# Performance work log

Measured on AMD Instinct MI355X. Metric: run time of the kernel, lower is better.

The kernel has to match this reference:

```python
import jax, jax.numpy as jnp
import numpy as np

B, SL, RATIO = 2, 2048, 16
SG = SL // RATIO          # 128 global tokens
S = SL + SG               # 2176 total sequence
D, H, NC, V = 512, 8, 2, 32000
HD, FF = D // H, 2 * D    # head_dim=64, dim_feedforward=2*d_model
K, R = 4, 4               # rel_pos_max_distance, local_attention_radius
NEG = -1e9


def _ln(x, g, b):
    m = x.mean(-1, keepdims=True)
    v = ((x - m) ** 2).mean(-1, keepdims=True)
    return (x - m) * jax.lax.rsqrt(v + 1e-5) * g + b


def _forward(token_ids, embed, global_token, rel_bias, q_w, q_b, k_w, k_b,
             v_w, v_b, o_w, o_b, ln1_g, ln1_b, ln2_g, ln2_b,
             ff1_w, ff1_b, ff2_w, ff2_b, cls_w1, cls_w2):
    pad = token_ids == 0                                   # B x Sl (padding_idx=0)
    x_long = embed[token_ids]                              # B x Sl x D
    seg_pad = pad.reshape(B, SG, RATIO).all(-1)            # B x Sg: segment fully padded
    x_global = jnp.broadcast_to(global_token, (B, SG, D))  # learned auxiliary global token
    x = jnp.concatenate([x_long, x_global], axis=1)        # B x S x D
    pad_all = jnp.concatenate([pad, seg_pad], axis=1)      # B x S

    # --- global-local attention structure (static masks) ---
    pos = jnp.arange(S)
    is_long = pos < SL
    both_long = is_long[:, None] & is_long[None, :]
    dist = pos[None, :] - pos[:, None]
    # long<->long restricted to local window; any pair involving a global token is allowed
    allowed = jnp.where(both_long, jnp.abs(dist) <= R, True)          # S x S
    rel = jnp.clip(dist, -K, K) + K                                   # S x S in [0, 2K]
    bias = jnp.where(both_long[None], rel_bias[:, rel], 0.0)          # H x S x S

    def heads(t):
        return t.reshape(B, S, H, HD).transpose(0, 2, 1, 3)           # B x H x S x hd
    q = heads(x @ q_w + q_b)
    k = heads(x @ k_w + k_b)
    v = heads(x @ v_w + v_b)
    logits = jnp.einsum('bhid,bhjd->bhij', q, k) / np.float32(np.sqrt(HD)) + bias[None]
    logits = jnp.where(allowed[None, None], logits, NEG)
    logits = jnp.where(pad_all[:, None, None, :], NEG, logits)        # key padding mask
    attn = jax.nn.softmax(logits, axis=-1)
    o = jnp.einsum('bhij,bhjd->bhid', attn, v).transpose(0, 2, 1, 3).reshape(B, S, D)

    # post-norm TransformerEncoderLayer (dropout=0, activation=relu)
    x = _ln(x + (o @ o_w + o_b), ln1_g, ln1_b)
    ff = jax.nn.relu(x @ ff1_w + ff1_b) @ ff2_w + ff2_b
    x = _ln(x + ff, ln2_g, ln2_b)

    # masked mean over global tokens, then MLP head
    zg = x[:, SL:, :]                                                 # B x Sg x D
    zg = jnp.where(seg_pad[..., None], 0.0, zg).sum(1) / (~seg_pad).sum(1, keepdims=True)
    return jax.nn.relu(zg @ cls_w1) @ cls_w2                          # B x Nc


def setup_inputs() -> dict:
    key = jax.random.key(0)
    ks = jax.random.split(key, 16)
    s = 0.02
    embed = jax.random.normal(ks[0], (V, D)) * s
    embed = embed.at[0].set(0.0)  # padding_idx row
    return {
        'x_long_token_ids': jax.random.randint(ks[1], (B, SL), 0, V),
        'embed': embed,
        'global_token': jax.random.normal(ks[2], (D,)) * s,
        'rel_bias': jax.random.normal(ks[3], (H, 2 * K + 1)) * s,
        'q_w': jax.random.normal(ks[4], (D, D)) * s, 'q_b': jnp.zeros((D,)),
        'k_w': jax.random.normal(ks[5], (D, D)) * s, 'k_b': jnp.zeros((D,)),
        'v_w': jax.random.normal(ks[6], (D, D)) * s, 'v_b': jnp.zeros((D,)),
        'o_w': jax.random.normal(ks[7], (D, D)) * s, 'o_b': jnp.zeros((D,)),
        'ln1_g': jnp.ones((D,)), 'ln1_b': jnp.zeros((D,)),
        'ln2_g': jnp.ones((D,)), 'ln2_b': jnp.zeros((D,)),
        'ff1_w': jax.random.normal(ks[8], (D, FF)) * s, 'ff1_b': jnp.zeros((FF,)),
        'ff2_w': jax.random.normal(ks[9], (FF, D)) * s, 'ff2_b': jnp.zeros((D,)),
        'cls_w1': jax.random.normal(ks[10], (D, D // 2)) * s,
        'cls_w2': jax.random.normal(ks[11], (D // 2, NC)) * s,
    }


def reference(x_long_token_ids, embed, global_token, rel_bias, q_w, q_b, k_w, k_b,
              v_w, v_b, o_w, o_b, ln1_g, ln1_b, ln2_g, ln2_b,
              ff1_w, ff1_b, ff2_w, ff2_b, cls_w1, cls_w2):
    return _forward(x_long_token_ids, embed, global_token, rel_bias, q_w, q_b,
                    k_w, k_b, v_w, v_b, o_w, o_b, ln1_g, ln1_b, ln2_g, ln2_b,
                    ff1_w, ff1_b, ff2_w, ff2_b, cls_w1, cls_w2)
```

## Files before the change

kernel.cpp:

```cpp
#include <hip/hip_runtime.h>
#include <hip/hip_bf16.h>
#include <cstddef>

#define B_ 2
#define SL_ 2048
#define RATIO_ 16
#define SG_ 128
#define S_ 2176
#define D_ 512
#define H_ 8
#define HD_ 64
#define FF_ 1024
#define NC_ 2
#define NEG_ (-1.0e9f)
#define MINF_ (-1.0e30f)
#define MROWS_ (B_ * S_)
#define GR_ (B_ * SG_)
#define KC_ 8

typedef __attribute__((ext_vector_type(8))) short short8;
typedef __attribute__((ext_vector_type(4))) float f32x4;

__device__ __forceinline__ void gll16(const void* g, void* l) {
    __builtin_amdgcn_global_load_lds((const __attribute__((address_space(1))) void*)g,
                                     (__attribute__((address_space(3))) void*)l, 16, 0, 0);
}
__device__ __forceinline__ unsigned short f2bf(float x) {
    __hip_bfloat16 h = __float2bfloat16(x);
    return *reinterpret_cast<unsigned short*>(&h);
}
__device__ __forceinline__ float wave_sum(float v) {
#pragma unroll
    for (int off = 1; off < 64; off <<= 1) v += __shfl_xor(v, off);
    return v;
}
#define BARRIER() do { asm volatile("" ::: "memory"); __builtin_amdgcn_s_barrier(); asm volatile("" ::: "memory"); } while (0)

__global__ void build_x_kernel(const int* __restrict__ ids,
                               const float* __restrict__ embed,
                               const float* __restrict__ gtok,
                               __hip_bfloat16* __restrict__ xb,
                               float* __restrict__ xg,
                               int* __restrict__ pad_all) {
    int row = blockIdx.x;
    int b = row / S_, s = row % S_;
    const float* src;
    if (s < SL_) {
        int tok = ids[b * SL_ + s];
        src = embed + (size_t)tok * D_;
        if (threadIdx.x == 0) pad_all[row] = (tok == 0) ? 1 : 0;
    } else {
        src = gtok;
        if (threadIdx.x == 0) {
            int g = s - SL_;
            int allz = 1;
            for (int r = 0; r < RATIO_; ++r)
                allz &= (ids[b * SL_ + g * RATIO_ + r] == 0) ? 1 : 0;
            pad_all[row] = allz;
        }
    }
    float4 v = ((const float4*)src)[threadIdx.x];
    __hip_bfloat16 hb[4] = {__float2bfloat16(v.x), __float2bfloat16(v.y),
                            __float2bfloat16(v.z), __float2bfloat16(v.w)};
    *(uint2*)(xb + (size_t)row * D_ + threadIdx.x * 4) = *(const uint2*)hb;
    if (s >= SL_)
        ((float4*)(xg + (size_t)(b * SG_ + s - SL_) * D_))[threadIdx.x] = v;
}

__global__ __launch_bounds__(256) void wt_all_kernel(const float* __restrict__ qw,
                                                     const float* __restrict__ kw,
                                                     const float* __restrict__ vw,
                                                     const float* __restrict__ ow,
                                                     const float* __restrict__ f1w,
                                                     const float* __restrict__ f2w,
                                                     __hip_bfloat16* __restrict__ WqT,
                                                     __hip_bfloat16* __restrict__ WkvT,
                                                     __hip_bfloat16* __restrict__ WoT,
                                                     __hip_bfloat16* __restrict__ W1T,
                                                     __hip_bfloat16* __restrict__ W2T,
                                                     const float* __restrict__ k_b,
                                                     const float* __restrict__ v_b,
                                                     float* __restrict__ kvb) {
    __shared__ float tile[64][65];
    int bid = blockIdx.x;
    int tid = threadIdx.x;
    if (bid == 0) {
#pragma unroll
        for (int i = tid; i < 1024; i += 256)
            kvb[i] = (i < 512) ? k_b[i] : v_b[i - 512];
    }
    const float* W; __hip_bfloat16* Wt; int K, N, tx, ty;
    if (bid < 192) {
        int which = bid >> 6, id = bid & 63;
        W = (which == 0) ? qw : (which == 1) ? kw : vw;
        Wt = (which == 0) ? WqT : (which == 1) ? WkvT : (WkvT + (size_t)512 * 512);
        K = 512; N = 512; tx = id & 7; ty = id >> 3;
    } else if (bid < 256) {
        int id = bid - 192; W = ow; Wt = WoT; K = 512; N = 512; tx = id & 7; ty = id >> 3;
    } else if (bid < 384) {
        int id = bid - 256; W = f1w; Wt = W1T; K = 512; N = 1024; tx = id & 15; ty = id >> 4;
    } else {
        int id = bid - 384; W = f2w; Wt = W2T; K = 1024; N = 512; tx = id & 7; ty = id >> 3;
    }
    int n0 = tx * 64, k0 = ty * 64;
    int c = tid & 63, r4 = tid >> 6;
#pragma unroll
    for (int i = 0; i < 16; ++i) {
        int r = i * 4 + r4;
        tile[r][c] = W[(size_t)(k0 + r) * N + n0 + c];
    }
    __syncthreads();
#pragma unroll
    for (int i = 0; i < 16; ++i) {
        int n = i * 4 + r4;
        Wt[(size_t)(n0 + n) * K + k0 + c] = __float2bfloat16(tile[c][n]);
    }
}

__global__ __launch_bounds__(256) void gemm_bt_kernel(const __hip_bfloat16* __restrict__ A,
                                                      const __hip_bfloat16* __restrict__ Bt,
                                                      const float* __restrict__ bias,
                                                      void* __restrict__ Cout,
                                                      int N, int K, int flags) {
    __shared__ short As[2][128 * 32];
    __shared__ short Bs[2][128 * 32];
    int tid = threadIdx.x;
    int m0 = blockIdx.y * 128, n0 = blockIdx.x * 128;
    int w = tid >> 6, lane = tid & 63;
    int wr = w >> 1, wc = w & 1;

    f32x4 acc[4][4];
#pragma unroll
    for (int m = 0; m < 4; ++m)
#pragma unroll
        for (int n = 0; n < 4; ++n)
            acc[m][n] = (f32x4){0.f, 0.f, 0.f, 0.f};

    int p0 = tid * 16, rs = p0 >> 6, cs = p0 & 63;
    const char* Ab = (const char*)A;
    const char* Bb = (const char*)Bt;

    auto STAGE = [&](int buf, int k0) {
        gll16(Ab + ((size_t)(m0 + rs) * K + k0) * 2 + cs, (char*)As[buf] + p0);
        gll16(Ab + ((size_t)(m0 + rs + 64) * K + k0) * 2 + cs, (char*)As[buf] + p0 + 4096);
        gll16(Bb + ((size_t)(n0 + rs) * K + k0) * 2 + cs, (char*)Bs[buf] + p0);
        gll16(Bb + ((size_t)(n0 + rs + 64) * K + k0) * 2 + cs, (char*)Bs[buf] + p0 + 4096);
    };
    STAGE(0, 0);
    int nk = K >> 5;
    for (int t = 0; t < nk; ++t) {
        int cur = t & 1;
        if (t + 1 < nk) {
            STAGE(cur ^ 1, (t + 1) << 5);
            asm volatile("s_waitcnt vmcnt(4)" ::: "memory");
        } else {
            asm volatile("s_waitcnt vmcnt(0)" ::: "memory");
        }
        BARRIER();
        short8 af[4], bfr[4];
#pragma unroll
        for (int m = 0; m < 4; ++m)
            af[m] = *(const short8*)&As[cur][(wr * 64 + m * 16 + (lane & 15)) * 32 + (lane >> 4) * 8];
#pragma unroll
        for (int n = 0; n < 4; ++n)
            bfr[n] = *(const short8*)&Bs[cur][(wc * 64 + n * 16 + (lane & 15)) * 32 + (lane >> 4) * 8];
#pragma unroll
        for (int m = 0; m < 4; ++m)
#pragma unroll
            for (int n = 0; n < 4; ++n)
                acc[m][n] = __builtin_amdgcn_mfma_f32_16x16x32_bf16(af[m], bfr[n], acc[m][n], 0, 0, 0);
        BARRIER();
    }

    int rbase = m0 + wr * 64 + (lane >> 4) * 4;
    int cbase = n0 + wc * 64 + (lane & 15);
#pragma unroll
    for (int m = 0; m < 4; ++m)
#pragma unroll
        for (int n = 0; n < 4; ++n) {
            int col = cbase + n * 16;
            float bv = bias[col];
#pragma unroll
            for (int j = 0; j < 4; ++j) {
                int row = rbase + m * 16 + j;
                float v = acc[m][n][j] + bv;
                if (flags & 1) v = fmaxf(v, 0.0f);
                if (flags & 2)
                    ((__hip_bfloat16*)Cout)[(size_t)row * N + col] = __float2bfloat16(v);
                else
                    ((float*)Cout)[(size_t)row * N + col] = v;
            }
        }
}

__global__ __launch_bounds__(256) void gemm64_kernel(const __hip_bfloat16* __restrict__ A,
                                                     const __hip_bfloat16* __restrict__ Bt,
                                                     const float* __restrict__ bias,
                                                     const float* __restrict__ Res,
                                                     void* __restrict__ Cout,
                                                     int N, int K, int flags) {
    __shared__ short As[2][64 * 32];
    __shared__ short Bs[2][64 * 32];
    int tid = threadIdx.x;
    int m0 = blockIdx.y * 64, n0 = blockIdx.x * 64;
    int w = tid >> 6, lane = tid & 63;
    int wr = w >> 1, wc = w & 1;

    f32x4 acc[2][2];
#pragma unroll
    for (int m = 0; m < 2; ++m)
#pragma unroll
        for (int n = 0; n < 2; ++n)
            acc[m][n] = (f32x4){0.f, 0.f, 0.f, 0.f};

    int p0 = tid * 16, rs = p0 >> 6, cs = p0 & 63;
    int rl = m0 + rs;
    size_t arow = (flags & 8) ? (size_t)((rl >> 7) * S_ + SL_ + (rl & 127)) : (size_t)rl;
    const char* Ab = (const char*)A;
    const char* Bb = (const char*)Bt;

    auto STAGE = [&](int buf, int k0) {
        gll16(Ab + (arow * K + k0) * 2 + cs, (char*)As[buf] + p0);
        gll16(Bb + ((size_t)(n0 + rs) * K + k0) * 2 + cs, (char*)Bs[buf] + p0);
    };
    STAGE(0, 0);
    int nk = K >> 5;
    for (int t = 0; t < nk; ++t) {
        int cur = t & 1;
        if (t + 1 < nk) {
            STAGE(cur ^ 1, (t + 1) << 5);
            asm volatile("s_waitcnt vmcnt(2)" ::: "memory");
        } else {
            asm volatile("s_waitcnt vmcnt(0)" ::: "memory");
        }
        BARRIER();
        short8 af[2], bfr[2];
#pragma unroll
        for (int m = 0; m < 2; ++m)
            af[m] = *(const short8*)&As[cur][(wr * 32 + m * 16 + (lane & 15)) * 32 + (lane >> 4) * 8];
#pragma unroll
        for (int n = 0; n < 2; ++n)
            bfr[n] = *(const short8*)&Bs[cur][(wc * 32 + n * 16 + (lane & 15)) * 32 + (lane >> 4) * 8];
#pragma unroll
        for (int m = 0; m < 2; ++m)
#pragma unroll
            for (int n = 0; n < 2; ++n)
                acc[m][n] = __builtin_amdgcn_mfma_f32_16x16x32_bf16(af[m], bfr[n], acc[m][n], 0, 0, 0);
        BARRIER();
    }

    int rbase = m0 + wr * 32 + (lane >> 4) * 4;
    int cbase = n0 + wc * 32 + (lane & 15);
#pragma unroll
    for (int m = 0; m < 2; ++m)
#pragma unroll
        for (int n = 0; n < 2; ++n) {
            int col = cbase + n * 16;
            float bv = bias[col];
#pragma unroll
            for (int j = 0; j < 4; ++j) {
                int row = rbase + m * 16 + j;
                float v = acc[m][n][j] + bv;
                if (flags & 4) v += Res[(size_t)row * N + col];
                if (flags & 1) v = fmaxf(v, 0.0f);
                if (flags & 2)
                    ((__hip_bfloat16*)Cout)[(size_t)row * N + col] = __float2bfloat16(v);
                else
                    ((float*)Cout)[(size_t)row * N + col] = v;
            }
        }
}

#define ATT_LDS_ 28480

__global__ __launch_bounds__(256, 4) void attn_global_kernel(const __hip_bfloat16* __restrict__ Qg,
                                                             const __hip_bfloat16* __restrict__ KV,
                                                             const int* __restrict__ pad_all,
                                                             float* __restrict__ pacc,
                                                             float* __restrict__ pm,
                                                             float* __restrict__ pl) {
    __shared__ __align__(16) char smem[ATT_LDS_];
    short* Qs = (short*)(smem + 0);
    short* Ks = (short*)(smem + 4608);
    short* Vt = (short*)(smem + 13824);
    short* Pl = (short*)(smem + 23040);
    float* padv = (float*)(smem + 27648);
    float* msh  = (float*)(smem + 27968);
    float* lsh  = (float*)(smem + 28224);
    float* Osh  = (float*)smem;

    const int TS[KC_ + 1] = {0, 4, 8, 12, 17, 21, 25, 29, 34};
    int bid = blockIdx.x;
    int c  = bid & 7;
    int qt = (bid >> 3) & 3;
    int h  = (bid >> 5) & 7;
    int b  = bid >> 8;
    int i0c = qt * 32;
    int tid = threadIdx.x;
    int w = tid >> 6, lane = tid & 63;
    int qg = w >> 1, kh = w & 1;
    int cq = lane & 15, g4 = lane >> 4;
    const int* pad = pad_all + b * S_;
    const short* qgp = (const short*)Qg;
    const short* kv  = (const short*)KV;

    {
        int q = tid >> 3, g = tid & 7;
        short8 v = *(const short8*)(qgp + (size_t)(b * SG_ + i0c + q) * D_ + h * HD_ + g * 8);
        *(short8*)(Qs + q * 72 + g * 8) = v;
    }

    float mreg = MINF_, lreg = 0.0f;
    f32x4 ot0 = {0,0,0,0}, ot1 = {0,0,0,0}, ot2 = {0,0,0,0}, ot3 = {0,0,0,0};

    for (int t = TS[c]; t < TS[c + 1]; ++t) {
        int j0 = t * 64;
        __syncthreads();
        {
            int key = tid >> 2, g2 = tid & 3;
            size_t base = (size_t)(b * S_ + j0 + key) * 1024 + h * HD_;
#pragma unroll
            for (int gg = 0; gg < 2; ++gg) {
                int g = g2 + gg * 4;
                short8 kvv = *(const short8*)(kv + base + g * 8);
                *(short8*)(Ks + key * 72 + g * 8) = kvv;
                short8 vv = *(const short8*)(kv + base + 512 + g * 8);
#pragma unroll
                for (int i = 0; i < 8; ++i)
                    Vt[(g * 8 + i) * 72 + key] = vv[i];
            }
            if (tid < 64) padv[tid] = pad[j0 + tid] ? NEG_ : 0.0f;
        }
        __syncthreads();

        short8 qf0 = *(const short8*)(Qs + (qg * 16 + cq) * 72 + 0 + g4 * 8);
        short8 qf1 = *(const short8*)(Qs + (qg * 16 + cq) * 72 + 32 + g4 * 8);
        f32x4 st0 = {0,0,0,0}, st1 = {0,0,0,0};
        {
            short8 kf;
            kf = *(const short8*)(Ks + (kh * 32 + cq) * 72 + 0 + g4 * 8);
            st0 = __builtin_amdgcn_mfma_f32_16x16x32_bf16(kf, qf0, st0, 0, 0, 0);
            kf = *(const short8*)(Ks + (kh * 32 + cq) * 72 + 32 + g4 * 8);
            st0 = __builtin_amdgcn_mfma_f32_16x16x32_bf16(kf, qf1, st0, 0, 0, 0);
            kf = *(const short8*)(Ks + (kh * 32 + 16 + cq) * 72 + 0 + g4 * 8);
            st1 = __builtin_amdgcn_mfma_f32_16x16x32_bf16(kf, qf0, st1, 0, 0, 0);
            kf = *(const short8*)(Ks + (kh * 32 + 16 + cq) * 72 + 32 + g4 * 8);
            st1 = __builtin_amdgcn_mfma_f32_16x16x32_bf16(kf, qf1, st1, 0, 0, 0);
        }
        float sarr[8];
#pragma unroll
        for (int mt = 0; mt < 2; ++mt)
#pragma unroll
            for (int j = 0; j < 4; ++j) {
                int k = kh * 32 + mt * 16 + g4 * 4 + j;
                sarr[mt * 4 + j] = (mt ? st1[j] : st0[j]) * 0.125f + padv[k];
            }
        float cmax = sarr[0];
#pragma unroll
        for (int i = 1; i < 8; ++i) cmax = fmaxf(cmax, sarr[i]);
        cmax = fmaxf(cmax, __shfl_xor(cmax, 16));
        cmax = fmaxf(cmax, __shfl_xor(cmax, 32));
        float mnew = fmaxf(mreg, cmax);
        float fac = __expf(mreg - mnew);
        float parr[8], psum = 0.0f;
#pragma unroll
        for (int i = 0; i < 8; ++i) { parr[i] = __expf(sarr[i] - mnew); psum += parr[i]; }
        psum += __shfl_xor(psum, 16);
        psum += __shfl_xor(psum, 32);
        lreg = lreg * fac + psum;
        mreg = mnew;
        ot0 *= fac; ot1 *= fac; ot2 *= fac; ot3 *= fac;
#pragma unroll
        for (int mt = 0; mt < 2; ++mt) {
            unsigned int lo = (unsigned int)f2bf(parr[mt * 4 + 0]) | ((unsigned int)f2bf(parr[mt * 4 + 1]) << 16);
            unsigned int hi = (unsigned int)f2bf(parr[mt * 4 + 2]) | ((unsigned int)f2bf(parr[mt * 4 + 3]) << 16);
            unsigned int* dst = (unsigned int*)(Pl + (qg * 16 + cq) * 72 + kh * 32 + mt * 16 + g4 * 4);
            dst[0] = lo; dst[1] = hi;
        }
        short8 pf = *(const short8*)(Pl + (qg * 16 + cq) * 72 + kh * 32 + g4 * 8);
        {
            short8 vf;
            vf = *(const short8*)(Vt + (0 * 16 + cq) * 72 + kh * 32 + g4 * 8);
            ot0 = __builtin_amdgcn_mfma_f32_16x16x32_bf16(vf, pf, ot0, 0, 0, 0);
            vf = *(const short8*)(Vt + (1 * 16 + cq) * 72 + kh * 32 + g4 * 8);
            ot1 = __builtin_amdgcn_mfma_f32_16x16x32_bf16(vf, pf, ot1, 0, 0, 0);
            vf = *(const short8*)(Vt + (2 * 16 + cq) * 72 + kh * 32 + g4 * 8);
            ot2 = __builtin_amdgcn_mfma_f32_16x16x32_bf16(vf, pf, ot2, 0, 0, 0);
            vf = *(const short8*)(Vt + (3 * 16 + cq) * 72 + kh * 32 + g4 * 8);
            ot3 = __builtin_amdgcn_mfma_f32_16x16x32_bf16(vf, pf, ot3, 0, 0, 0);
        }
    }

    __syncthreads();
    if (g4 == 0) {
        msh[(qg * 2 + kh) * 16 + cq] = mreg;
        lsh[(qg * 2 + kh) * 16 + cq] = lreg;
    }
    __syncthreads();
    {
        float m0 = msh[(qg * 2 + 0) * 16 + cq], m1 = msh[(qg * 2 + 1) * 16 + cq];
        float Mm = fmaxf(m0, m1);
        float e_self = __expf(mreg - Mm);
        f32x4 o;
        o = ot0 * e_self; *(f32x4*)(Osh + ((qg * 2 + kh) * 16 + cq) * 68 + 0  + g4 * 4) = o;
        o = ot1 * e_self; *(f32x4*)(Osh + ((qg * 2 + kh) * 16 + cq) * 68 + 16 + g4 * 4) = o;
        o = ot2 * e_self; *(f32x4*)(Osh + ((qg * 2 + kh) * 16 + cq) * 68 + 32 + g4 * 4) = o;
        o = ot3 * e_self; *(f32x4*)(Osh + ((qg * 2 + kh) * 16 + cq) * 68 + 48 + g4 * 4) = o;
    }
    __syncthreads();
    {
        int q_all = tid >> 3, d0 = (tid & 7) * 8;
        int qg2 = q_all >> 4, ql = q_all & 15;
        float mm0 = msh[(qg2 * 2 + 0) * 16 + ql], mm1 = msh[(qg2 * 2 + 1) * 16 + ql];
        float MM = fmaxf(mm0, mm1);
        float lt = lsh[(qg2 * 2 + 0) * 16 + ql] * __expf(mm0 - MM) +
                   lsh[(qg2 * 2 + 1) * 16 + ql] * __expf(mm1 - MM);
        int prow = ((c * B_ + b) * H_ + h) * SG_ + qt * 32 + q_all;
#pragma unroll
        for (int i = 0; i < 8; ++i) {
            float a = Osh[((qg2 * 2 + 0) * 16 + ql) * 68 + d0 + i] +
                      Osh[((qg2 * 2 + 1) * 16 + ql) * 68 + d0 + i];
            pacc[(size_t)prow * HD_ + d0 + i] = a;
        }
        if ((tid & 7) == 0) { pm[prow] = MM; pl[prow] = lt; }
    }
}

__global__ __launch_bounds__(256) void attn_combine_kernel(const float* __restrict__ pacc,
                                                           const float* __restrict__ pm,
                                                           const float* __restrict__ pl,
                                                           __hip_bfloat16* __restrict__ Og) {
    int wave = (int)((blockIdx.x * (size_t)blockDim.x + threadIdx.x) >> 6);
    int lane = threadIdx.x & 63;
    int gq = wave & (SG_ - 1);
    int h  = (wave >> 7) & 7;
    int b  = wave >> 10;

    float M = MINF_;
#pragma unroll
    for (int c = 0; c < KC_; ++c) {
        int pidx = ((c * B_ + b) * H_ + h) * SG_ + gq;
        M = fmaxf(M, pm[pidx]);
    }
    float L = 0.0f, Ov = 0.0f;
#pragma unroll
    for (int c = 0; c < KC_; ++c) {
        int pidx = ((c * B_ + b) * H_ + h) * SG_ + gq;
        float e = __expf(pm[pidx] - M);
        L += pl[pidx] * e;
        Ov += pacc[(size_t)pidx * HD_ + lane] * e;
    }
    Og[(size_t)(b * SG_ + gq) * D_ + h * HD_ + lane] = __float2bfloat16(Ov / L);
}

__global__ __launch_bounds__(256) void ln_kernel(const float* __restrict__ A,
                                                 const float* __restrict__ g,
                                                 const float* __restrict__ be,
                                                 float* __restrict__ out,
                                                 __hip_bfloat16* __restrict__ outb,
                                                 int wb) {
    int row = blockIdx.x;
    int tid = threadIdx.x;
    size_t base = (size_t)row * D_;
    float x0 = A[base + tid];
    float x1 = A[base + tid + 256];
    float s1 = x0 + x1;
    float s2 = x0 * x0 + x1 * x1;
    for (int off = 1; off < 64; off <<= 1) {
        s1 += __shfl_xor(s1, off);
        s2 += __shfl_xor(s2, off);
    }
    __shared__ float ws1[4], ws2[4];
    int wid = tid >> 6;
    if ((tid & 63) == 0) { ws1[wid] = s1; ws2[wid] = s2; }
    __syncthreads();
    s1 = ws1[0] + ws1[1] + ws1[2] + ws1[3];
    s2 = ws2[0] + ws2[1] + ws2[2] + ws2[3];
    float mean = s1 * (1.0f / D_);
    float var  = s2 * (1.0f / D_) - mean * mean;
    float rstd = rsqrtf(var + 1e-5f);
    float o0 = (x0 - mean) * rstd * g[tid]       + be[tid];
    float o1 = (x1 - mean) * rstd * g[tid + 256] + be[tid + 256];
    out[base + tid]       = o0;
    out[base + tid + 256] = o1;
    if (wb) {
        outb[base + tid]       = __float2bfloat16(o0);
        outb[base + tid + 256] = __float2bfloat16(o1);
    }
}

__global__ __launch_bounds__(256) void cls_part_kernel(const float* __restrict__ x2g,
                                                       const int* __restrict__ pad_all,
                                                       const float* __restrict__ w1,
                                                       float* __restrict__ part) {
    int kc = blockIdx.x, b = blockIdx.y, tid = threadIdx.x;
    __shared__ float wrow[SG_];
    __shared__ float zpart[4][64];
    __shared__ float zgs[64];
    if (tid < SG_) wrow[tid] = pad_all[b * S_ + SL_ + tid] ? 0.0f : 1.0f;
    __syncthreads();

    int j = tid & 63, grp = tid >> 6;
    float a = 0.0f;
#pragma unroll 8
    for (int g = grp; g < SG_; g += 4)
        a = fmaf(wrow[g], x2g[(size_t)(b * SG_ + g) * D_ + kc * 64 + j], a);
    zpart[grp][j] = a;
    __syncthreads();
    if (tid < 64) {
        float cnt = 0.0f;
#pragma unroll 16
        for (int g = 0; g < SG_; ++g) cnt += wrow[g];
        zgs[tid] = (zpart[0][tid] + zpart[1][tid] + zpart[2][tid] + zpart[3][tid]) / cnt;
    }
    __syncthreads();

    float s = 0.0f;
#pragma unroll 8
    for (int d = 0; d < 64; ++d)
        s = fmaf(zgs[d], w1[(size_t)(kc * 64 + d) * 256 + tid], s);
    part[(b * 8 + kc) * 256 + tid] = s;
}

__global__ __launch_bounds__(256) void cls_fin_kernel(const float* __restrict__ part,
                                                      const float* __restrict__ w2,
                                                      float* __restrict__ out) {
    int b = blockIdx.x, n = threadIdx.x;
    float hsum = 0.0f;
#pragma unroll
    for (int kc = 0; kc < 8; ++kc) hsum += part[(b * 8 + kc) * 256 + n];
    hsum = fmaxf(hsum, 0.0f);
    float o0 = hsum * w2[(size_t)n * NC_ + 0];
    float o1 = hsum * w2[(size_t)n * NC_ + 1];
    o0 = wave_sum(o0);
    o1 = wave_sum(o1);
    __shared__ float r0[4], r1[4];
    if ((n & 63) == 0) { r0[n >> 6] = o0; r1[n >> 6] = o1; }
    __syncthreads();
    if (n == 0) {
        out[b * NC_ + 0] = r0[0] + r0[1] + r0[2] + r0[3];
        out[b * NC_ + 1] = r1[0] + r1[1] + r1[2] + r1[3];
    }
}

extern "C" void kernel_launch(void* const* d_in, const int* in_sizes, int n_in,
                              void* d_out, int out_size, void* d_ws, size_t ws_size,
                              hipStream_t stream) {
    const int*   ids    = (const int*)d_in[0];
    const float* embed  = (const float*)d_in[1];
    const float* gtok   = (const float*)d_in[2];
    const float* q_w    = (const float*)d_in[4];
    const float* q_b    = (const float*)d_in[5];
    const float* k_w    = (const float*)d_in[6];
    const float* k_b    = (const float*)d_in[7];
    const float* v_w    = (const float*)d_in[8];
    const float* v_b    = (const float*)d_in[9];
    const float* o_w    = (const float*)d_in[10];
    const float* o_b    = (const float*)d_in[11];
    const float* ln1_g  = (const float*)d_in[12];
    const float* ln1_b  = (const float*)d_in[13];
    const float* ln2_g  = (const float*)d_in[14];
    const float* ln2_b  = (const float*)d_in[15];
    const float* ff1_w  = (const float*)d_in[16];
    const float* ff1_b  = (const float*)d_in[17];
    const float* ff2_w  = (const float*)d_in[18];
    const float* ff2_b  = (const float*)d_in[19];
    const float* cls_w1 = (const float*)d_in[20];
    const float* cls_w2 = (const float*)d_in[21];

    char* ws = (char*)d_ws;
    __hip_bfloat16* x_b     = (__hip_bfloat16*)(ws + 0);
    __hip_bfloat16* kv_bf   = (__hip_bfloat16*)(ws + 4456448);
    __hip_bfloat16* qg_bf   = (__hip_bfloat16*)(ws + 13369344);
    __hip_bfloat16* og_bf   = (__hip_bfloat16*)(ws + 13631488);
    float*          xg_f32  = (float*)(ws + 13893632);
    float*          tmpA    = (float*)(ws + 14417920);
    float*          x1g     = (float*)(ws + 14942208);
    __hip_bfloat16* x1g_b   = (__hip_bfloat16*)(ws + 15466496);
    __hip_bfloat16* ffh_b   = (__hip_bfloat16*)(ws + 15728640);
    float*          tmpB    = (float*)(ws + 16252928);
    float*          x2g     = (float*)(ws + 16777216);
    __hip_bfloat16* WqT     = (__hip_bfloat16*)(ws + 17301504);
    __hip_bfloat16* WkvT    = (__hip_bfloat16*)(ws + 17825792);
    __hip_bfloat16* WoT     = (__hip_bfloat16*)(ws + 18874368);
    __hip_bfloat16* W1T     = (__hip_bfloat16*)(ws + 19398656);
    __hip_bfloat16* W2T     = (__hip_bfloat16*)(ws + 20447232);
    float*          kvb     = (float*)(ws + 21495808);
    int*            pad_all = (int*)(ws + 21499904);
    float*          pacc    = (float*)(ws + 21520384);
    float*          pm      = (float*)(ws + 25714688);
    float*          pl      = (float*)(ws + 25780224);
    float*          clspart = (float*)(ws + 25845760);

    build_x_kernel<<<MROWS_, 128, 0, stream>>>(ids, embed, gtok, x_b, xg_f32, pad_all);
    wt_all_kernel<<<512, 256, 0, stream>>>(q_w, k_w, v_w, o_w, ff1_w, ff2_w,
                                           WqT, WkvT, WoT, W1T, W2T, k_b, v_b, kvb);

    gemm_bt_kernel<<<dim3(8, 34), 256, 0, stream>>>(x_b, WkvT, kvb, kv_bf, 1024, 512, 2);
    gemm64_kernel<<<dim3(8, 4), 256, 0, stream>>>(x_b, WqT, q_b, nullptr, qg_bf, 512, 512, 2 | 8);

    attn_global_kernel<<<512, 256, 0, stream>>>(qg_bf, kv_bf, pad_all, pacc, pm, pl);
    attn_combine_kernel<<<512, 256, 0, stream>>>(pacc, pm, pl, og_bf);

    gemm64_kernel<<<dim3(8, 4), 256, 0, stream>>>(og_bf, WoT, o_b, xg_f32, tmpA, 512, 512, 4);
    ln_kernel<<<GR_, 256, 0, stream>>>(tmpA, ln1_g, ln1_b, x1g, x1g_b, 1);
    gemm64_kernel<<<dim3(16, 4), 256, 0, stream>>>(x1g_b, W1T, ff1_b, nullptr, ffh_b, 1024, 512, 1 | 2);
    gemm64_kernel<<<dim3(8, 4), 256, 0, stream>>>(ffh_b, W2T, ff2_b, x1g, tmpB, 512, 1024, 4);
    ln_kernel<<<GR_, 256, 0, stream>>>(tmpB, ln2_g, ln2_b, x2g, nullptr, 0);

    cls_part_kernel<<<dim3(8, B_), 256, 0, stream>>>(x2g, pad_all, cls_w1, clspart);
    cls_fin_kernel<<<B_, 256, 0, stream>>>(clspart, cls_w2, (float*)d_out);
}
```

Before: 102.1 us.

## Merge prep and QKV launches, fuse tail stages into one cooperative kernel

Merges the embedding build and the weight transpose into one prep kernel, and merges the KV and global-Q GEMMs into one launch. Replaces the seven tail launches (attention combine, O-proj, LN1, FF1, FF2, LN2, classifier part and final) with a single 64-block cooperative kernel that separates stages with grid syncs. The aim is to cut launch overhead and inter-kernel gaps across many tiny kernels. In exchange, the tail now runs on only 64 blocks, and each grid sync adds its own latency.

```diff
diff --git a/kernel.cpp b/kernel.cpp
--- a/kernel.cpp
+++ b/kernel.cpp
@@ -1,6 +1,9 @@
 #include <hip/hip_runtime.h>
 #include <hip/hip_bf16.h>
+#include <hip/hip_cooperative_groups.h>
 #include <cstddef>
+
+namespace cg = cooperative_groups;
 
 #define B_ 2
 #define SL_ 2048
@@ -36,71 +39,72 @@
 }
 #define BARRIER() do { asm volatile("" ::: "memory"); __builtin_amdgcn_s_barrier(); asm volatile("" ::: "memory"); } while (0)
 
-__global__ void build_x_kernel(const int* __restrict__ ids,
-                               const float* __restrict__ embed,
-                               const float* __restrict__ gtok,
-                               __hip_bfloat16* __restrict__ xb,
-                               float* __restrict__ xg,
-                               int* __restrict__ pad_all) {
-    int row = blockIdx.x;
-    int b = row / S_, s = row % S_;
-    const float* src;
-    if (s < SL_) {
-        int tok = ids[b * SL_ + s];
-        src = embed + (size_t)tok * D_;
-        if (threadIdx.x == 0) pad_all[row] = (tok == 0) ? 1 : 0;
-    } else {
-        src = gtok;
-        if (threadIdx.x == 0) {
-            int g = s - SL_;
-            int allz = 1;
-            for (int r = 0; r < RATIO_; ++r)
-                allz &= (ids[b * SL_ + g * RATIO_ + r] == 0) ? 1 : 0;
-            pad_all[row] = allz;
-        }
-    }
-    float4 v = ((const float4*)src)[threadIdx.x];
-    __hip_bfloat16 hb[4] = {__float2bfloat16(v.x), __float2bfloat16(v.y),
-                            __float2bfloat16(v.z), __float2bfloat16(v.w)};
-    *(uint2*)(xb + (size_t)row * D_ + threadIdx.x * 4) = *(const uint2*)hb;
-    if (s >= SL_)
-        ((float4*)(xg + (size_t)(b * SG_ + s - SL_) * D_))[threadIdx.x] = v;
-}
-
-__global__ __launch_bounds__(256) void wt_all_kernel(const float* __restrict__ qw,
-                                                     const float* __restrict__ kw,
-                                                     const float* __restrict__ vw,
-                                                     const float* __restrict__ ow,
-                                                     const float* __restrict__ f1w,
-                                                     const float* __restrict__ f2w,
-                                                     __hip_bfloat16* __restrict__ WqT,
-                                                     __hip_bfloat16* __restrict__ WkvT,
-                                                     __hip_bfloat16* __restrict__ WoT,
-                                                     __hip_bfloat16* __restrict__ W1T,
-                                                     __hip_bfloat16* __restrict__ W2T,
-                                                     const float* __restrict__ k_b,
-                                                     const float* __restrict__ v_b,
-                                                     float* __restrict__ kvb) {
+__global__ __launch_bounds__(256) void prep_kernel(const int* __restrict__ ids,
+                                                   const float* __restrict__ embed,
+                                                   const float* __restrict__ gtok,
+                                                   __hip_bfloat16* __restrict__ xb,
+                                                   float* __restrict__ xg,
+                                                   int* __restrict__ pad_all,
+                                                   const float* __restrict__ qw,
+                                                   const float* __restrict__ kw,
+                                                   const float* __restrict__ vw,
+                                                   const float* __restrict__ ow,
+                                                   const float* __restrict__ f1w,
+                                                   const float* __restrict__ f2w,
+                                                   __hip_bfloat16* __restrict__ WqT,
+                                                   __hip_bfloat16* __restrict__ WkvT,
+                                                   __hip_bfloat16* __restrict__ WoT,
+                                                   __hip_bfloat16* __restrict__ W1T,
+                                                   __hip_bfloat16* __restrict__ W2T,
+                                                   const float* __restrict__ k_b,
+                                                   const float* __restrict__ v_b,
+                                                   float* __restrict__ kvb) {
     __shared__ float tile[64][65];
-    int bid = blockIdx.x;
-    int tid = threadIdx.x;
-    if (bid == 0) {
-#pragma unroll
+    int bid = blockIdx.x, tid = threadIdx.x;
+    if (bid < 2176) {
+        int half = tid >> 7, lt = tid & 127;
+        int row = bid * 2 + half;
+        int b = row / S_, s = row % S_;
+        const float* src;
+        if (s < SL_) {
+            int tok = ids[b * SL_ + s];
+            src = embed + (size_t)tok * D_;
+            if (lt == 0) pad_all[row] = (tok == 0) ? 1 : 0;
+        } else {
+            src = gtok;
+            if (lt == 0) {
+                int g = s - SL_;
+                int allz = 1;
+                for (int r = 0; r < RATIO_; ++r)
+                    allz &= (ids[b * SL_ + g * RATIO_ + r] == 0) ? 1 : 0;
+                pad_all[row] = allz;
+            }
+        }
+        float4 v = ((const float4*)src)[lt];
+        __hip_bfloat16 hb[4] = {__float2bfloat16(v.x), __float2bfloat16(v.y),
+                                __float2bfloat16(v.z), __float2bfloat16(v.w)};
+        *(uint2*)(xb + (size_t)row * D_ + lt * 4) = *(const uint2*)hb;
+        if (s >= SL_)
+            ((float4*)(xg + (size_t)(b * SG_ + s - SL_) * D_))[lt] = v;
+        return;
+    }
+    int wbid = bid - 2176;
+    if (wbid == 0) {
         for (int i = tid; i < 1024; i += 256)
             kvb[i] = (i < 512) ? k_b[i] : v_b[i - 512];
     }
     const float* W; __hip_bfloat16* Wt; int K, N, tx, ty;
-    if (bid < 192) {
-        int which = bid >> 6, id = bid & 63;
+    if (wbid < 192) {
+        int which = wbid >> 6, id = wbid & 63;
         W = (which == 0) ? qw : (which == 1) ? kw : vw;
         Wt = (which == 0) ? WqT : (which == 1) ? WkvT : (WkvT + (size_t)512 * 512);
         K = 512; N = 512; tx = id & 7; ty = id >> 3;
-    } else if (bid < 256) {
-        int id = bid - 192; W = ow; Wt = WoT; K = 512; N = 512; tx = id & 7; ty = id >> 3;
-    } else if (bid < 384) {
-        int id = bid - 256; W = f1w; Wt = W1T; K = 512; N = 1024; tx = id & 15; ty = id >> 4;
+    } else if (wbid < 256) {
+        int id = wbid - 192; W = ow; Wt = WoT; K = 512; N = 512; tx = id & 7; ty = id >> 3;
+    } else if (wbid < 384) {
+        int id = wbid - 256; W = f1w; Wt = W1T; K = 512; N = 1024; tx = id & 15; ty = id >> 4;
     } else {
-        int id = bid - 384; W = f2w; Wt = W2T; K = 1024; N = 512; tx = id & 7; ty = id >> 3;
+        int id = wbid - 384; W = f2w; Wt = W2T; K = 1024; N = 512; tx = id & 7; ty = id >> 3;
     }
     int n0 = tx * 64, k0 = ty * 64;
     int c = tid & 63, r4 = tid >> 6;
@@ -117,158 +121,132 @@
     }
 }
 
-__global__ __launch_bounds__(256) void gemm_bt_kernel(const __hip_bfloat16* __restrict__ A,
-                                                      const __hip_bfloat16* __restrict__ Bt,
-                                                      const float* __restrict__ bias,
-                                                      void* __restrict__ Cout,
-                                                      int N, int K, int flags) {
-    __shared__ short As[2][128 * 32];
-    __shared__ short Bs[2][128 * 32];
-    int tid = threadIdx.x;
-    int m0 = blockIdx.y * 128, n0 = blockIdx.x * 128;
+__global__ __launch_bounds__(256) void qkv_kernel(const __hip_bfloat16* __restrict__ x_b,
+                                                  const __hip_bfloat16* __restrict__ WkvT,
+                                                  const float* __restrict__ kvb,
+                                                  __hip_bfloat16* __restrict__ kv_bf,
+                                                  const __hip_bfloat16* __restrict__ WqT,
+                                                  const float* __restrict__ q_b,
+                                                  __hip_bfloat16* __restrict__ qg_bf) {
+    __shared__ short SA[2][4096];
+    __shared__ short SB[2][4096];
+    int bid = blockIdx.x, tid = threadIdx.x;
     int w = tid >> 6, lane = tid & 63;
     int wr = w >> 1, wc = w & 1;
-
-    f32x4 acc[4][4];
-#pragma unroll
-    for (int m = 0; m < 4; ++m)
-#pragma unroll
-        for (int n = 0; n < 4; ++n)
-            acc[m][n] = (f32x4){0.f, 0.f, 0.f, 0.f};
-
     int p0 = tid * 16, rs = p0 >> 6, cs = p0 & 63;
-    const char* Ab = (const char*)A;
-    const char* Bb = (const char*)Bt;
-
-    auto STAGE = [&](int buf, int k0) {
-        gll16(Ab + ((size_t)(m0 + rs) * K + k0) * 2 + cs, (char*)As[buf] + p0);
-        gll16(Ab + ((size_t)(m0 + rs + 64) * K + k0) * 2 + cs, (char*)As[buf] + p0 + 4096);
-        gll16(Bb + ((size_t)(n0 + rs) * K + k0) * 2 + cs, (char*)Bs[buf] + p0);
-        gll16(Bb + ((size_t)(n0 + rs + 64) * K + k0) * 2 + cs, (char*)Bs[buf] + p0 + 4096);
-    };
-    STAGE(0, 0);
-    int nk = K >> 5;
-    for (int t = 0; t < nk; ++t) {
-        int cur = t & 1;
-        if (t + 1 < nk) {
-            STAGE(cur ^ 1, (t + 1) << 5);
-            asm volatile("s_waitcnt vmcnt(4)" ::: "memory");
-        } else {
-            asm volatile("s_waitcnt vmcnt(0)" ::: "memory");
-        }
-        BARRIER();
-        short8 af[4], bfr[4];
+
+    if (bid < 272) {
+        const int K = 512, N = 1024;
+        int m0 = (bid >> 3) * 128, n0 = (bid & 7) * 128;
+        f32x4 acc[4][4];
 #pragma unroll
         for (int m = 0; m < 4; ++m)
-            af[m] = *(const short8*)&As[cur][(wr * 64 + m * 16 + (lane & 15)) * 32 + (lane >> 4) * 8];
-#pragma unroll
-        for (int n = 0; n < 4; ++n)
-            bfr[n] = *(const short8*)&Bs[cur][(wc * 64 + n * 16 + (lane & 15)) * 32 + (lane >> 4) * 8];
+#pragma unroll
+            for (int n = 0; n < 4; ++n) acc[m][n] = (f32x4){0.f, 0.f, 0.f, 0.f};
+        const char* Ab = (const char*)x_b;
+        const char* Bb = (const char*)WkvT;
+        auto STAGE = [&](int buf, int k0) {
+            gll16(Ab + ((size_t)(m0 + rs) * K + k0) * 2 + cs, (char*)SA[buf] + p0);
+            gll16(Ab + ((size_t)(m0 + rs + 64) * K + k0) * 2 + cs, (char*)SA[buf] + p0 + 4096);
+            gll16(Bb + ((size_t)(n0 + rs) * K + k0) * 2 + cs, (char*)SB[buf] + p0);
+            gll16(Bb + ((size_t)(n0 + rs + 64) * K + k0) * 2 + cs, (char*)SB[buf] + p0 + 4096);
+        };
+        STAGE(0, 0);
+        const int nk = K >> 5;
+        for (int t = 0; t < nk; ++t) {
+            int cur = t & 1;
+            if (t + 1 < nk) {
+                STAGE(cur ^ 1, (t + 1) << 5);
+                asm volatile("s_waitcnt vmcnt(4)" ::: "memory");
+            } else {
+                asm volatile("s_waitcnt vmcnt(0)" ::: "memory");
+            }
+            BARRIER();
+            short8 af[4], bfr[4];
+#pragma unroll
+            for (int m = 0; m < 4; ++m)
+                af[m] = *(const short8*)&SA[cur][(wr * 64 + m * 16 + (lane & 15)) * 32 + (lane >> 4) * 8];
+#pragma unroll
+            for (int n = 0; n < 4; ++n)
+                bfr[n] = *(const short8*)&SB[cur][(wc * 64 + n * 16 + (lane & 15)) * 32 + (lane >> 4) * 8];
+#pragma unroll
+            for (int m = 0; m < 4; ++m)
+#pragma unroll
+                for (int n = 0; n < 4; ++n)
+                    acc[m][n] = __builtin_amdgcn_mfma_f32_16x16x32_bf16(af[m], bfr[n], acc[m][n], 0, 0, 0);
+            BARRIER();
+        }
+        int rbase = m0 + wr * 64 + (lane >> 4) * 4;
+        int cbase = n0 + wc * 64 + (lane & 15);
 #pragma unroll
         for (int m = 0; m < 4; ++m)
 #pragma unroll
-            for (int n = 0; n < 4; ++n)
-                acc[m][n] = __builtin_amdgcn_mfma_f32_16x16x32_bf16(af[m], bfr[n], acc[m][n], 0, 0, 0);
-        BARRIER();
-    }
-
-    int rbase = m0 + wr * 64 + (lane >> 4) * 4;
-    int cbase = n0 + wc * 64 + (lane & 15);
-#pragma unroll
-    for (int m = 0; m < 4; ++m)
-#pragma unroll
-        for (int n = 0; n < 4; ++n) {
-            int col = cbase + n * 16;
-            float bv = bias[col];
-#pragma unroll
-            for (int j = 0; j < 4; ++j) {
-                int row = rbase + m * 16 + j;
-                float v = acc[m][n][j] + bv;
-                if (flags & 1) v = fmaxf(v, 0.0f);
-                if (flags & 2)
-                    ((__hip_bfloat16*)Cout)[(size_t)row * N + col] = __float2bfloat16(v);
-                else
-                    ((float*)Cout)[(size_t)row * N + col] = v;
-            }
-        }
-}
-
-__global__ __launch_bounds__(256) void gemm64_kernel(const __hip_bfloat16* __restrict__ A,
-                                                     const __hip_bfloat16* __restrict__ Bt,
-                                                     const float* __restrict__ bias,
-                                                     const float* __restrict__ Res,
-                                                     void* __restrict__ Cout,
-                                                     int N, int K, int flags) {
-    __shared__ short As[2][64 * 32];
-    __shared__ short Bs[2][64 * 32];
-    int tid = threadIdx.x;
-    int m0 = blockIdx.y * 64, n0 = blockIdx.x * 64;
-    int w = tid >> 6, lane = tid & 63;
-    int wr = w >> 1, wc = w & 1;
-
-    f32x4 acc[2][2];
-#pragma unroll
-    for (int m = 0; m < 2; ++m)
-#pragma unroll
-        for (int n = 0; n < 2; ++n)
-            acc[m][n] = (f32x4){0.f, 0.f, 0.f, 0.f};
-
-    int p0 = tid * 16, rs = p0 >> 6, cs = p0 & 63;
-    int rl = m0 + rs;
-    size_t arow = (flags & 8) ? (size_t)((rl >> 7) * S_ + SL_ + (rl & 127)) : (size_t)rl;
-    const char* Ab = (const char*)A;
-    const char* Bb = (const char*)Bt;
-
-    auto STAGE = [&](int buf, int k0) {
-        gll16(Ab + (arow * K + k0) * 2 + cs, (char*)As[buf] + p0);
-        gll16(Bb + ((size_t)(n0 + rs) * K + k0) * 2 + cs, (char*)Bs[buf] + p0);
-    };
-    STAGE(0, 0);
-    int nk = K >> 5;
-    for (int t = 0; t < nk; ++t) {
-        int cur = t & 1;
-        if (t + 1 < nk) {
-            STAGE(cur ^ 1, (t + 1) << 5);
-            asm volatile("s_waitcnt vmcnt(2)" ::: "memory");
-        } else {
-            asm volatile("s_waitcnt vmcnt(0)" ::: "memory");
-        }
-        BARRIER();
-        short8 af[2], bfr[2];
+            for (int n = 0; n < 4; ++n) {
+                int col = cbase + n * 16;
+                float bv = kvb[col];
+#pragma unroll
+                for (int j = 0; j < 4; ++j) {
+                    int row = rbase + m * 16 + j;
+                    kv_bf[(size_t)row * N + col] = __float2bfloat16(acc[m][n][j] + bv);
+                }
+            }
+    } else {
+        const int K = 512, N = 512;
+        int idx = bid - 272;
+        int m0 = (idx >> 3) * 64, n0 = (idx & 7) * 64;
+        f32x4 acc[2][2];
 #pragma unroll
         for (int m = 0; m < 2; ++m)
-            af[m] = *(const short8*)&As[cur][(wr * 32 + m * 16 + (lane & 15)) * 32 + (lane >> 4) * 8];
-#pragma unroll
-        for (int n = 0; n < 2; ++n)
-            bfr[n] = *(const short8*)&Bs[cur][(wc * 32 + n * 16 + (lane & 15)) * 32 + (lane >> 4) * 8];
+#pragma unroll
+            for (int n = 0; n < 2; ++n) acc[m][n] = (f32x4){0.f, 0.f, 0.f, 0.f};
+        int rl = m0 + rs;
+        size_t arow = (size_t)((rl >> 7) * S_ + SL_ + (rl & 127));
+        const char* Ab = (const char*)x_b;
+        const char* Bb = (const char*)WqT;
+        auto STAGE = [&](int buf, int k0) {
+            gll16(Ab + (arow * K + k0) * 2 + cs, (char*)SA[buf] + p0);
+            gll16(Bb + ((size_t)(n0 + rs) * K + k0) * 2 + cs, (char*)SB[buf] + p0);
+        };
+        STAGE(0, 0);
+        const int nk = K >> 5;
+        for (int t = 0; t < nk; ++t) {
+            int cur = t & 1;
+            if (t + 1 < nk) {
+                STAGE(cur ^ 1, (t + 1) << 5);
+                asm volatile("s_waitcnt vmcnt(2)" ::: "memory");
+            } else {
+                asm volatile("s_waitcnt vmcnt(0)" ::: "memory");
+            }
+            BARRIER();
+            short8 af[2], bfr[2];
+#pragma unroll
+            for (int m = 0; m < 2; ++m)
+                af[m] = *(const short8*)&SA[cur][(wr * 32 + m * 16 + (lane & 15)) * 32 + (lane >> 4) * 8];
+#pragma unroll
+            for (int n = 0; n < 2; ++n)
+                bfr[n] = *(const short8*)&SB[cur][(wc * 32 + n * 16 + (lane & 15)) * 32 + (lane >> 4) * 8];
+#pragma unroll
+            for (int m = 0; m < 2; ++m)
+#pragma unroll
+                for (int n = 0; n < 2; ++n)
+                    acc[m][n] = __builtin_amdgcn_mfma_f32_16x16x32_bf16(af[m], bfr[n], acc[m][n], 0, 0, 0);
+            BARRIER();
+        }
+        int rbase = m0 + wr * 32 + (lane >> 4) * 4;
+        int cbase = n0 + wc * 32 + (lane & 15);
 #pragma unroll
         for (int m = 0; m < 2; ++m)
 #pragma unroll
-            for (int n = 0; n < 2; ++n)
-                acc[m][n] = __builtin_amdgcn_mfma_f32_16x16x32_bf16(af[m], bfr[n], acc[m][n], 0, 0, 0);
-        BARRIER();
-    }
-
-    int rbase = m0 + wr * 32 + (lane >> 4) * 4;
-    int cbase = n0 + wc * 32 + (lane & 15);
-#pragma unroll
-    for (int m = 0; m < 2; ++m)
-#pragma unroll
-        for (int n = 0; n < 2; ++n) {
-            int col = cbase + n * 16;
-            float bv = bias[col];
-#pragma unroll
-            for (int j = 0; j < 4; ++j) {
-                int row = rbase + m * 16 + j;
-                float v = acc[m][n][j] + bv;
-                if (flags & 4) v += Res[(size_t)row * N + col];
-                if (flags & 1) v = fmaxf(v, 0.0f);
-                if (flags & 2)
-                    ((__hip_bfloat16*)Cout)[(size_t)row * N + col] = __float2bfloat16(v);
-                else
-                    ((float*)Cout)[(size_t)row * N + col] = v;
-            }
-        }
+            for (int n = 0; n < 2; ++n) {
+                int col = cbase + n * 16;
+                float bv = q_b[col];
+#pragma unroll
+                for (int j = 0; j < 4; ++j) {
+                    int row = rbase + m * 16 + j;
+                    qg_bf[(size_t)row * N + col] = __float2bfloat16(acc[m][n][j] + bv);
+                }
+            }
+    }
 }
 
 #define ATT_LDS_ 28480
@@ -426,51 +404,84 @@
     }
 }
 
-__global__ __launch_bounds__(256) void attn_combine_kernel(const float* __restrict__ pacc,
-                                                           const float* __restrict__ pm,
-                                                           const float* __restrict__ pl,
-                                                           __hip_bfloat16* __restrict__ Og) {
-    int wave = (int)((blockIdx.x * (size_t)blockDim.x + threadIdx.x) >> 6);
-    int lane = threadIdx.x & 63;
-    int gq = wave & (SG_ - 1);
-    int h  = (wave >> 7) & 7;
-    int b  = wave >> 10;
-
-    float M = MINF_;
-#pragma unroll
-    for (int c = 0; c < KC_; ++c) {
-        int pidx = ((c * B_ + b) * H_ + h) * SG_ + gq;
-        M = fmaxf(M, pm[pidx]);
-    }
-    float L = 0.0f, Ov = 0.0f;
-#pragma unroll
-    for (int c = 0; c < KC_; ++c) {
-        int pidx = ((c * B_ + b) * H_ + h) * SG_ + gq;
-        float e = __expf(pm[pidx] - M);
-        L += pl[pidx] * e;
-        Ov += pacc[(size_t)pidx * HD_ + lane] * e;
-    }
-    Og[(size_t)(b * SG_ + gq) * D_ + h * HD_ + lane] = __float2bfloat16(Ov / L);
-}
-
-__global__ __launch_bounds__(256) void ln_kernel(const float* __restrict__ A,
-                                                 const float* __restrict__ g,
-                                                 const float* __restrict__ be,
-                                                 float* __restrict__ out,
-                                                 __hip_bfloat16* __restrict__ outb,
-                                                 int wb) {
-    int row = blockIdx.x;
+__device__ __forceinline__ void gemm64_body(short (&As)[2][2048], short (&Bs)[2][2048],
+                                            const __hip_bfloat16* A, const __hip_bfloat16* Bt,
+                                            const float* bias, const float* Res, void* Cout,
+                                            int N, int K, int flags, int m0, int n0) {
+    int tid = threadIdx.x;
+    int w = tid >> 6, lane = tid & 63;
+    int wr = w >> 1, wc = w & 1;
+    f32x4 acc[2][2];
+#pragma unroll
+    for (int m = 0; m < 2; ++m)
+#pragma unroll
+        for (int n = 0; n < 2; ++n) acc[m][n] = (f32x4){0.f, 0.f, 0.f, 0.f};
+    int p0 = tid * 16, rs = p0 >> 6, cs = p0 & 63;
+    const char* Ab = (const char*)A;
+    const char* Bb = (const char*)Bt;
+    auto STAGE = [&](int buf, int k0) {
+        gll16(Ab + ((size_t)(m0 + rs) * K + k0) * 2 + cs, (char*)As[buf] + p0);
+        gll16(Bb + ((size_t)(n0 + rs) * K + k0) * 2 + cs, (char*)Bs[buf] + p0);
+    };
+    STAGE(0, 0);
+    int nk = K >> 5;
+    for (int t = 0; t < nk; ++t) {
+        int cur = t & 1;
+        if (t + 1 < nk) {
+            STAGE(cur ^ 1, (t + 1) << 5);
+            asm volatile("s_waitcnt vmcnt(2)" ::: "memory");
+        } else {
+            asm volatile("s_waitcnt vmcnt(0)" ::: "memory");
+        }
+        BARRIER();
+        short8 af[2], bfr[2];
+#pragma unroll
+        for (int m = 0; m < 2; ++m)
+            af[m] = *(const short8*)&As[cur][(wr * 32 + m * 16 + (lane & 15)) * 32 + (lane >> 4) * 8];
+#pragma unroll
+        for (int n = 0; n < 2; ++n)
+            bfr[n] = *(const short8*)&Bs[cur][(wc * 32 + n * 16 + (lane & 15)) * 32 + (lane >> 4) * 8];
+#pragma unroll
+        for (int m = 0; m < 2; ++m)
+#pragma unroll
+            for (int n = 0; n < 2; ++n)
+                acc[m][n] = __builtin_amdgcn_mfma_f32_16x16x32_bf16(af[m], bfr[n], acc[m][n], 0, 0, 0);
+        BARRIER();
+    }
+    int rbase = m0 + wr * 32 + (lane >> 4) * 4;
+    int cbase = n0 + wc * 32 + (lane & 15);
+#pragma unroll
+    for (int m = 0; m < 2; ++m)
+#pragma unroll
+        for (int n = 0; n < 2; ++n) {
+            int col = cbase + n * 16;
+            float bv = bias[col];
+#pragma unroll
+            for (int j = 0; j < 4; ++j) {
+                int row = rbase + m * 16 + j;
+                float v = acc[m][n][j] + bv;
+                if (flags & 4) v += Res[(size_t)row * N + col];
+                if (flags & 1) v = fmaxf(v, 0.0f);
+                if (flags & 2)
+                    ((__hip_bfloat16*)Cout)[(size_t)row * N + col] = __float2bfloat16(v);
+                else
+                    ((float*)Cout)[(size_t)row * N + col] = v;
+            }
+        }
+}
+
+__device__ __forceinline__ void ln_row(const float* A, const float* g, const float* be,
+                                       float* out, __hip_bfloat16* outb, int wb, int row,
+                                       float* ws1, float* ws2) {
     int tid = threadIdx.x;
     size_t base = (size_t)row * D_;
     float x0 = A[base + tid];
     float x1 = A[base + tid + 256];
-    float s1 = x0 + x1;
-    float s2 = x0 * x0 + x1 * x1;
+    float s1 = x0 + x1, s2 = x0 * x0 + x1 * x1;
     for (int off = 1; off < 64; off <<= 1) {
         s1 += __shfl_xor(s1, off);
         s2 += __shfl_xor(s2, off);
     }
-    __shared__ float ws1[4], ws2[4];
     int wid = tid >> 6;
     if ((tid & 63) == 0) { ws1[wid] = s1; ws2[wid] = s2; }
     __syncthreads();
@@ -487,59 +498,118 @@
         outb[base + tid]       = __float2bfloat16(o0);
         outb[base + tid + 256] = __float2bfloat16(o1);
     }
-}
-
-__global__ __launch_bounds__(256) void cls_part_kernel(const float* __restrict__ x2g,
-                                                       const int* __restrict__ pad_all,
-                                                       const float* __restrict__ w1,
-                                                       float* __restrict__ part) {
-    int kc = blockIdx.x, b = blockIdx.y, tid = threadIdx.x;
+    __syncthreads();
+}
+
+struct TailP {
+    const float* pacc; const float* pm; const float* pl;
+    __hip_bfloat16* og;
+    const __hip_bfloat16* WoT; const float* o_b; const float* xg; float* tmpA;
+    const float* ln1_g; const float* ln1_b; float* x1g; __hip_bfloat16* x1g_b;
+    const __hip_bfloat16* W1T; const float* ff1_b; __hip_bfloat16* ffh;
+    const __hip_bfloat16* W2T; const float* ff2_b; float* tmpB;
+    const float* ln2_g; const float* ln2_b; float* x2g;
+    const int* pad_all; const float* w1; float* part; const float* w2; float* out;
+};
+
+__global__ __launch_bounds__(256) void tail_kernel(TailP p) {
+    cg::grid_group gg = cg::this_grid();
+    __shared__ short TA[2][2048];
+    __shared__ short TB[2][2048];
+    __shared__ float ws1[4], ws2[4];
     __shared__ float wrow[SG_];
     __shared__ float zpart[4][64];
     __shared__ float zgs[64];
-    if (tid < SG_) wrow[tid] = pad_all[b * S_ + SL_ + tid] ? 0.0f : 1.0f;
-    __syncthreads();
-
-    int j = tid & 63, grp = tid >> 6;
-    float a = 0.0f;
+    __shared__ float r0s[4], r1s[4];
+    int bid = blockIdx.x, tid = threadIdx.x;
+
+    {
+        int wave_g = bid * 4 + (tid >> 6);
+        int lane = tid & 63;
+#pragma unroll
+        for (int i = 0; i < 8; ++i) {
+            int item = wave_g * 8 + i;
+            int gq = item & (SG_ - 1);
+            int h  = (item >> 7) & 7;
+            int b  = item >> 10;
+            float M = MINF_;
+#pragma unroll
+            for (int c = 0; c < KC_; ++c)
+                M = fmaxf(M, p.pm[((c * B_ + b) * H_ + h) * SG_ + gq]);
+            float L = 0.0f, Ov = 0.0f;
+#pragma unroll
+            for (int c = 0; c < KC_; ++c) {
+                int pidx = ((c * B_ + b) * H_ + h) * SG_ + gq;
+                float e = __expf(p.pm[pidx] - M);
+                L += p.pl[pidx] * e;
+                Ov += p.pacc[(size_t)pidx * HD_ + lane] * e;
+            }
+            p.og[(size_t)(b * SG_ + gq) * D_ + h * HD_ + lane] = __float2bfloat16(Ov / L);
+        }
+    }
+    __threadfence(); gg.sync();
+
+    if (bid < 32)
+        gemm64_body(TA, TB, p.og, p.WoT, p.o_b, p.xg, p.tmpA, 512, 512, 4, (bid >> 3) * 64, (bid & 7) * 64);
+    __threadfence(); gg.sync();
+
+    for (int r = 0; r < 4; ++r)
+        ln_row(p.tmpA, p.ln1_g, p.ln1_b, p.x1g, p.x1g_b, 1, bid * 4 + r, ws1, ws2);
+    __threadfence(); gg.sync();
+
+    gemm64_body(TA, TB, p.x1g_b, p.W1T, p.ff1_b, nullptr, p.ffh, 1024, 512, 1 | 2, (bid >> 4) * 64, (bid & 15) * 64);
+    __threadfence(); gg.sync();
+
+    if (bid < 32)
+        gemm64_body(TA, TB, p.ffh, p.W2T, p.ff2_b, p.x1g, p.tmpB, 512, 1024, 4, (bid >> 3) * 64, (bid & 7) * 64);
+    __threadfence(); gg.sync();
+
+    for (int r = 0; r < 4; ++r)
+        ln_row(p.tmpB, p.ln2_g, p.ln2_b, p.x2g, nullptr, 0, bid * 4 + r, ws1, ws2);
+    __threadfence(); gg.sync();
+
+    if (bid < 16) {
+        int kc = bid & 7, b = bid >> 3;
+        if (tid < SG_) wrow[tid] = p.pad_all[b * S_ + SL_ + tid] ? 0.0f : 1.0f;
+        __syncthreads();
+        int j = tid & 63, grp = tid >> 6;
+        float a = 0.0f;
 #pragma unroll 8
-    for (int g = grp; g < SG_; g += 4)
-        a = fmaf(wrow[g], x2g[(size_t)(b * SG_ + g) * D_ + kc * 64 + j], a);
-    zpart[grp][j] = a;
-    __syncthreads();
-    if (tid < 64) {
-        float cnt = 0.0f;
+        for (int g = grp; g < SG_; g += 4)
+            a = fmaf(wrow[g], p.x2g[(size_t)(b * SG_ + g) * D_ + kc * 64 + j], a);
+        zpart[grp][j] = a;
+        __syncthreads();
+        if (tid < 64) {
+            float cnt = 0.0f;
 #pragma unroll 16
-        for (int g = 0; g < SG_; ++g) cnt += wrow[g];
-        zgs[tid] = (zpart[0][tid] + zpart[1][tid] + zpart[2][tid] + zpart[3][tid]) / cnt;
-    }
-    __syncthreads();
-
-    float s = 0.0f;
+            for (int g = 0; g < SG_; ++g) cnt += wrow[g];
+            zgs[tid] = (zpart[0][tid] + zpart[1][tid] + zpart[2][tid] + zpart[3][tid]) / cnt;
+        }
+        __syncthreads();
+        float s = 0.0f;
 #pragma unroll 8
-    for (int d = 0; d < 64; ++d)
-        s = fmaf(zgs[d], w1[(size_t)(kc * 64 + d) * 256 + tid], s);
-    part[(b * 8 + kc) * 256 + tid] = s;
-}
-
-__global__ __launch_bounds__(256) void cls_fin_kernel(const float* __restrict__ part,
-                                                      const float* __restrict__ w2,
-                                                      float* __restrict__ out) {
-    int b = blockIdx.x, n = threadIdx.x;
-    float hsum = 0.0f;
-#pragma unroll
-    for (int kc = 0; kc < 8; ++kc) hsum += part[(b * 8 + kc) * 256 + n];
-    hsum = fmaxf(hsum, 0.0f);
-    float o0 = hsum * w2[(size_t)n * NC_ + 0];
-    float o1 = hsum * w2[(size_t)n * NC_ + 1];
-    o0 = wave_sum(o0);
-    o1 = wave_sum(o1);
-    __shared__ float r0[4], r1[4];
-    if ((n & 63) == 0) { r0[n >> 6] = o0; r1[n >> 6] = o1; }
-    __syncthreads();
-    if (n == 0) {
-        out[b * NC_ + 0] = r0[0] + r0[1] + r0[2] + r0[3];
-        out[b * NC_ + 1] = r1[0] + r1[1] + r1[2] + r1[3];
+        for (int d = 0; d < 64; ++d)
+            s = fmaf(zgs[d], p.w1[(size_t)(kc * 64 + d) * 256 + tid], s);
+        p.part[(b * 8 + kc) * 256 + tid] = s;
+    }
+    __threadfence(); gg.sync();
+
+    if (bid < 2) {
+        int b = bid;
+        float hsum = 0.0f;
+#pragma unroll
+        for (int kc = 0; kc < 8; ++kc) hsum += p.part[(b * 8 + kc) * 256 + tid];
+        hsum = fmaxf(hsum, 0.0f);
+        float o0 = hsum * p.w2[(size_t)tid * NC_ + 0];
+        float o1 = hsum * p.w2[(size_t)tid * NC_ + 1];
+        o0 = wave_sum(o0);
+        o1 = wave_sum(o1);
+        if ((tid & 63) == 0) { r0s[tid >> 6] = o0; r1s[tid >> 6] = o1; }
+        __syncthreads();
+        if (tid == 0) {
+            p.out[b * NC_ + 0] = r0s[0] + r0s[1] + r0s[2] + r0s[3];
+            p.out[b * NC_ + 1] = r1s[0] + r1s[1] + r1s[2] + r1s[3];
+        }
     }
 }
 
@@ -592,22 +662,24 @@
     float*          pl      = (float*)(ws + 25780224);
     float*          clspart = (float*)(ws + 25845760);
 
-    build_x_kernel<<<MROWS_, 128, 0, stream>>>(ids, embed, gtok, x_b, xg_f32, pad_all);
-    wt_all_kernel<<<512, 256, 0, stream>>>(q_w, k_w, v_w, o_w, ff1_w, ff2_w,
-                                           WqT, WkvT, WoT, W1T, W2T, k_b, v_b, kvb);
-
-    gemm_bt_kernel<<<dim3(8, 34), 256, 0, stream>>>(x_b, WkvT, kvb, kv_bf, 1024, 512, 2);
-    gemm64_kernel<<<dim3(8, 4), 256, 0, stream>>>(x_b, WqT, q_b, nullptr, qg_bf, 512, 512, 2 | 8);
+    prep_kernel<<<2688, 256, 0, stream>>>(ids, embed, gtok, x_b, xg_f32, pad_all,
+                                          q_w, k_w, v_w, o_w, ff1_w, ff2_w,
+                                          WqT, WkvT, WoT, W1T, W2T, k_b, v_b, kvb);
+
+    qkv_kernel<<<304, 256, 0, stream>>>(x_b, WkvT, kvb, kv_bf, WqT, q_b, qg_bf);
 
     attn_global_kernel<<<512, 256, 0, stream>>>(qg_bf, kv_bf, pad_all, pacc, pm, pl);
-    attn_combine_kernel<<<512, 256, 0, stream>>>(pacc, pm, pl, og_bf);
-
-    gemm64_kernel<<<dim3(8, 4), 256, 0, stream>>>(og_bf, WoT, o_b, xg_f32, tmpA, 512, 512, 4);
-    ln_kernel<<<GR_, 256, 0, stream>>>(tmpA, ln1_g, ln1_b, x1g, x1g_b, 1);
-    gemm64_kernel<<<dim3(16, 4), 256, 0, stream>>>(x1g_b, W1T, ff1_b, nullptr, ffh_b, 1024, 512, 1 | 2);
-    gemm64_kernel<<<dim3(8, 4), 256, 0, stream>>>(ffh_b, W2T, ff2_b, x1g, tmpB, 512, 1024, 4);
-    ln_kernel<<<GR_, 256, 0, stream>>>(tmpB, ln2_g, ln2_b, x2g, nullptr, 0);
-
-    cls_part_kernel<<<dim3(8, B_), 256, 0, stream>>>(x2g, pad_all, cls_w1, clspart);
-    cls_fin_kernel<<<B_, 256, 0, stream>>>(clspart, cls_w2, (float*)d_out);
-}
+
+    TailP tp;
+    tp.pacc = pacc; tp.pm = pm; tp.pl = pl;
+    tp.og = og_bf;
+    tp.WoT = WoT; tp.o_b = o_b; tp.xg = xg_f32; tp.tmpA = tmpA;
+    tp.ln1_g = ln1_g; tp.ln1_b = ln1_b; tp.x1g = x1g; tp.x1g_b = x1g_b;
+    tp.W1T = W1T; tp.ff1_b = ff1_b; tp.ffh = ffh_b;
+    tp.W2T = W2T; tp.ff2_b = ff2_b; tp.tmpB = tmpB;
+    tp.ln2_g = ln2_g; tp.ln2_b = ln2_b; tp.x2g = x2g;
+    tp.pad_all = pad_all; tp.w1 = cls_w1; tp.part = clspart; tp.w2 = cls_w2;
+    tp.out = (float*)d_out;
+    void* kargs[] = {(void*)&tp};
+    hipLaunchCooperativeKernel((void*)tail_kernel, dim3(64), dim3(256), kargs, 0, stream);
+}
```

New measurement: 194.1 us. 1.9x slower.
